# Kernel tuning notes

Measured on AMD Instinct MI355X. Metric: run time of the kernel, lower is better.

## Reference

```python
import jax, jax.numpy as jnp
import numpy as np

B, T, E, H = 16, 4096, 64, 8
K, GADD, RADD, REGION = 256, 8, 8, 64
MIN_SIGMA, SIGMA_SCALE, SIGMA_BOOST = 0.05, 1.0, 2.0
VS = K * (4 + GADD + RADD)


def setup_inputs() -> dict:
    key = jax.random.key(0)
    ks = jax.random.split(key, 10)
    return {
        "x": jax.random.normal(ks[0], (B, T, E), jnp.float32),
        "Wq": jax.random.normal(ks[1], (E, E * H), jnp.float32) / np.float32(np.sqrt(E)),
        "Wk": jax.random.normal(ks[2], (E, E * H), jnp.float32) / np.float32(np.sqrt(E)),
        "Wv": jax.random.normal(ks[3], (E, E * H), jnp.float32) / np.float32(np.sqrt(E)),
        "Wu": jax.random.normal(ks[4], (H * E, E), jnp.float32) / np.float32(np.sqrt(H * E)),
        "bu": jnp.zeros((E,), jnp.float32),
        "means_p": jax.random.normal(ks[5], (K, 2), jnp.float32),
        "sigmas_p": jax.random.normal(ks[6], (K,), jnp.float32),
        "global_ints": jax.random.randint(ks[7], (B, 1, K, GADD, 2), 0, T, jnp.int32),
        "local_offsets": jax.random.randint(ks[8], (B, 1, K, RADD, 2), 0, REGION, jnp.int32),
    }


def _flip(x):
    # util.flip: sort each (i, j) pair so row >= col (below-diagonal / causal)
    hi = jnp.max(x, axis=-1, keepdims=True)
    lo = jnp.min(x, axis=-1, keepdims=True)
    return jnp.concatenate([hi, lo], axis=-1)


def _forward(x, Wq, Wk, Wv, Wu, bu, means_p, sigmas_p, global_ints, local_offsets):
    b, t, e = x.shape
    h, k = H, K

    # ---- hyper(): continuous means/sigmas over the (t, t) attention matrix
    means = jnp.broadcast_to(means_p[None, None], (b, 1, k, 2))
    means = _flip(means)
    means = jax.nn.sigmoid(means) * (t - 1)                       # (b,1,k,2) in [0, t-1]
    sig = jax.nn.softplus(sigmas_p + SIGMA_BOOST) + MIN_SIGMA     # (k,)
    sigmas = jnp.broadcast_to((sig * t * SIGMA_SCALE)[None, None, :, None], (b, 1, k, 2))

    # ---- ngenerate: 2^rank floor/ceil neighbours + global + relative-window samples
    fl, ce = jnp.floor(means), jnp.ceil(means)
    pat = jnp.array([[0., 0.], [0., 1.], [1., 0.], [1., 1.]], jnp.float32)  # (4,2)
    neigh = fl[:, :, :, None, :] * (1.0 - pat) + ce[:, :, :, None, :] * pat
    neigh = jnp.clip(neigh, 0, t - 1).astype(jnp.int32)           # (b,1,k,4,2)
    lower = jnp.clip(jnp.floor(means) - REGION // 2, 0, t - REGION).astype(jnp.int32)
    local = lower[:, :, :, None, :] + local_offsets               # (b,1,k,RADD,2)
    idx = jnp.concatenate([neigh, global_ints, local], axis=3).reshape(b, 1, VS, 2)
    idx = _flip(idx)                                              # (b,1,VS,2), row >= col

    # ---- densities: unnormalized Gaussian weight of each int tuple under each point
    indfl = idx.astype(jnp.float32)
    diff = (indfl[:, :, :, None, :] - means[:, :, None, :, :]) / sigmas[:, :, None, :, :]
    props = jnp.exp(-0.5 * jnp.sum(diff * diff, axis=-1))         # (b,1,VS,K)

    # ---- nduplicates: zero all-but-one of identical index tuples per batch
    ids = idx[:, 0, :, 0] * t + idx[:, 0, :, 1]                   # (b, VS)
    def dupmask(v):
        o = jnp.argsort(v)
        s = v[o]
        d = jnp.concatenate([jnp.zeros((1,), bool), s[1:] == s[:-1]])
        return jnp.zeros((VS,), bool).at[o].set(d)
    dups = jax.vmap(dupmask)(ids)                                  # (b, VS)
    props = jnp.where(dups[:, None, :, None], 0.0, props)
    props = props / jnp.sum(props, axis=2, keepdims=True)
    weights = jnp.sum(props, axis=3)                               # mvalues == 1 -> (b,1,VS)

    # ---- Q/K/V projections, per-head dim = e
    scale = e ** -0.25
    q = (x @ Wq).reshape(b, t, h, e).transpose(0, 2, 1, 3).reshape(b * h, t, e) * scale
    kk = (x @ Wk).reshape(b, t, h, e).transpose(0, 2, 1, 3).reshape(b * h, t, e) * scale
    v = (x @ Wv).reshape(b, t, h, e).transpose(0, 2, 1, 3).reshape(b * h, t, e)

    rows = jnp.broadcast_to(idx[:, 0, None, :, 0], (b, h, VS)).reshape(b * h, VS)
    cols = jnp.broadcast_to(idx[:, 0, None, :, 1], (b, h, VS)).reshape(b * h, VS)
    w = jnp.broadcast_to(weights[:, 0, None, :], (b, h, VS)).reshape(b * h, VS)

    sq = jnp.take_along_axis(q, rows[:, :, None], axis=1)          # (b*h, VS, e)
    sk = jnp.take_along_axis(kk, cols[:, :, None], axis=1)
    dot = w * jnp.sum(sq * sk, axis=-1)                            # (b*h, VS)

    # ---- segment (row-wise) softmax over the sparse pattern
    seg = (jnp.arange(b * h, dtype=jnp.int32)[:, None] * t + rows).reshape(-1)
    dflat = dot.reshape(-1)
    m = jax.lax.stop_gradient(jax.ops.segment_max(dflat, seg, num_segments=b * h * t))
    ex = jnp.exp(dflat - m[seg])
    ssum = jax.ops.segment_sum(ex, seg, num_segments=b * h * t)
    p = ex / ssum[seg]                                             # (b*h*VS,)

    # ---- sparse batched matmul: scatter-add p * V[col] into rows
    gathered = jnp.take_along_axis(v, cols[:, :, None], axis=1).reshape(-1, e)
    out = jax.ops.segment_sum(p[:, None] * gathered, seg, num_segments=b * h * t)
    out = out.reshape(b, h, t, e).transpose(0, 2, 1, 3).reshape(b, t, h * e)
    return out @ Wu + bu


def reference(x, Wq, Wk, Wv, Wu, bu, means_p, sigmas_p, global_ints, local_offsets):
    return _forward(x, Wq, Wk, Wv, Wu, bu, means_p, sigmas_p, global_ints, local_offsets)
```

## Files before the change

kernel.cpp:

```cpp
#include <hip/hip_runtime.h>
#include <hip/hip_bf16.h>
#include <math.h>

#define B 16
#define T 4096
#define E 64
#define H 8
#define KP 256
#define GADD 8
#define RADD 8
#define REGION 64
#define VS (KP * (4 + GADD + RADD))
#define NH (H * E)
#define NCHUNK 20
#define HSZ 16384

typedef __attribute__((ext_vector_type(8))) short bf16x8;
typedef __attribute__((ext_vector_type(4))) float f32x4;

__device__ inline ushort f2bf(float f) {
    union { __hip_bfloat16 h; ushort u; } cv;
    cv.h = __float2bfloat16(f);
    return cv.u;
}
__device__ inline float bflo(uint32_t p) { return __uint_as_float(p << 16); }
__device__ inline float bfhi(uint32_t p) { return __uint_as_float(p & 0xffff0000u); }

__global__ void k_points(const float* __restrict__ means_p, const float* __restrict__ sigmas_p,
                         float* __restrict__ meansf, float* __restrict__ sigt) {
    int k = threadIdx.x;
    if (k >= KP) return;
    float a = means_p[2 * k], b = means_p[2 * k + 1];
    float hi = fmaxf(a, b), lo = fminf(a, b);
    meansf[2 * k]     = (1.f / (1.f + expf(-hi))) * (float)(T - 1);
    meansf[2 * k + 1] = (1.f / (1.f + expf(-lo))) * (float)(T - 1);
    float sp = sigmas_p[k] + 2.0f;
    float s = (sp > 20.f) ? sp : log1pf(expf(sp));
    sigt[k] = (s + 0.05f) * (float)T;
}

__global__ void k_wvu(const float* __restrict__ Wv, const float* __restrict__ Wu,
                      float* __restrict__ Wvu) {
    int idx = blockIdx.x * blockDim.x + threadIdx.x;
    if (idx >= E * NH) return;
    int i = idx / NH, c = idx % NH;
    int h = c / E, j = c % E;
    float acc = 0.f;
    for (int d = 0; d < E; ++d)
        acc += Wv[i * NH + h * E + d] * Wu[(h * E + d) * E + j];
    Wvu[i * NH + c] = acc;
}

__global__ void k_prep_x(const float* __restrict__ x, ushort* __restrict__ xb) {
    int i = (blockIdx.x * 256 + threadIdx.x) * 8;
    float4 a = *(const float4*)(x + i);
    float4 b = *(const float4*)(x + i + 4);
    uint4 r;
    r.x = (uint32_t)f2bf(a.x) | ((uint32_t)f2bf(a.y) << 16);
    r.y = (uint32_t)f2bf(a.z) | ((uint32_t)f2bf(a.w) << 16);
    r.z = (uint32_t)f2bf(b.x) | ((uint32_t)f2bf(b.y) << 16);
    r.w = (uint32_t)f2bf(b.z) | ((uint32_t)f2bf(b.w) << 16);
    *(uint4*)(xb + i) = r;
}

__global__ void k_prep_w(const float* __restrict__ Wq, const float* __restrict__ Wk,
                         const float* __restrict__ Wvu, ushort* __restrict__ wfrag) {
    int t = blockIdx.x * 256 + threadIdx.x;
    if (t >= 3 * 32 * 2 * 64) return;
    int lane = t & 63, kf = (t >> 6) & 1, nf = (t >> 7) & 31, z = t >> 12;
    const float* W = (z == 0) ? Wq : (z == 1) ? Wk : Wvu;
    int col = nf * 16 + (lane & 15);
    int krow = kf * 32 + (lane >> 4) * 8;
    uint4 r;
    uint32_t v[8];
    #pragma unroll
    for (int j = 0; j < 8; ++j) v[j] = f2bf(W[(size_t)(krow + j) * NH + col]);
    r.x = v[0] | (v[1] << 16); r.y = v[2] | (v[3] << 16);
    r.z = v[4] | (v[5] << 16); r.w = v[6] | (v[7] << 16);
    *(uint4*)(wfrag + (size_t)t * 8) = r;
}

__global__ __launch_bounds__(256) void k_proj(const ushort* __restrict__ xb,
        const ushort* __restrict__ wfrag,
        __hip_bfloat16* __restrict__ q, __hip_bfloat16* __restrict__ kk,
        __hip_bfloat16* __restrict__ vu) {
    int z = blockIdx.y;
    __hip_bfloat16* outp = (z == 0) ? q : (z == 1) ? kk : vu;
    int row0 = blockIdx.x * 64;
    int wv = threadIdx.x >> 6, lane = threadIdx.x & 63;
    int arow = lane & 15, akoff = (lane >> 4) * 8;

    bf16x8 bfr[8][2];
    #pragma unroll
    for (int nf = 0; nf < 8; ++nf) {
        size_t base = ((size_t)((z * 32 + wv * 8 + nf) * 2) * 64 + lane) * 8;
        bfr[nf][0] = *(const bf16x8*)(wfrag + base);
        bfr[nf][1] = *(const bf16x8*)(wfrag + base + 64 * 8);
    }

    #pragma unroll
    for (int mf = 0; mf < 4; ++mf) {
        bf16x8 a0 = *(const bf16x8*)(xb + (size_t)(row0 + mf * 16 + arow) * 64 + akoff);
        bf16x8 a1 = *(const bf16x8*)(xb + (size_t)(row0 + mf * 16 + arow) * 64 + 32 + akoff);
        f32x4 acc[8];
        #pragma unroll
        for (int nf = 0; nf < 8; ++nf) {
            f32x4 t = {0.f, 0.f, 0.f, 0.f};
            t = __builtin_amdgcn_mfma_f32_16x16x32_bf16(a0, bfr[nf][0], t, 0, 0, 0);
            t = __builtin_amdgcn_mfma_f32_16x16x32_bf16(a1, bfr[nf][1], t, 0, 0, 0);
            acc[nf] = t;
        }
        int rbase = row0 + mf * 16 + (lane >> 4) * 4;
        #pragma unroll
        for (int rg = 0; rg < 4; ++rg) {
            uint4 o;
            o.x = (uint32_t)f2bf(acc[0][rg]) | ((uint32_t)f2bf(acc[1][rg]) << 16);
            o.y = (uint32_t)f2bf(acc[2][rg]) | ((uint32_t)f2bf(acc[3][rg]) << 16);
            o.z = (uint32_t)f2bf(acc[4][rg]) | ((uint32_t)f2bf(acc[5][rg]) << 16);
            o.w = (uint32_t)f2bf(acc[6][rg]) | ((uint32_t)f2bf(acc[7][rg]) << 16);
            *(uint4*)((ushort*)outp + (size_t)(rbase + rg) * NH + wv * 128 + (lane & 15) * 8) = o;
        }
    }
}

__global__ void k_build_idx(const int* __restrict__ g_ints, const int* __restrict__ l_offs,
                            const float* __restrict__ meansf,
                            int* __restrict__ idxrow, int* __restrict__ idxcol,
                            int* __restrict__ hkey, int* __restrict__ hval) {
    int b = blockIdx.y;
    int s = blockIdx.x * 256 + threadIdx.x;
    int* keys = hkey + b * HSZ;
    int* vals = hval + b * HSZ;
    int k = s / 20, slot = s % 20;
    float m0 = meansf[2 * k], m1 = meansf[2 * k + 1];
    int i0, i1;
    if (slot < 4) {
        float a  = (slot & 2) ? ceilf(m0) : floorf(m0);
        float bb = (slot & 1) ? ceilf(m1) : floorf(m1);
        a  = fminf(fmaxf(a, 0.f), (float)(T - 1));
        bb = fminf(fmaxf(bb, 0.f), (float)(T - 1));
        i0 = (int)a; i1 = (int)bb;
    } else if (slot < 12) {
        const int* p = g_ints + ((size_t)((b * KP + k) * GADD) + (slot - 4)) * 2;
        i0 = p[0]; i1 = p[1];
    } else {
        int lo0 = (int)fminf(fmaxf(floorf(m0) - (float)(REGION / 2), 0.f), (float)(T - REGION));
        int lo1 = (int)fminf(fmaxf(floorf(m1) - (float)(REGION / 2), 0.f), (float)(T - REGION));
        const int* p = l_offs + ((size_t)((b * KP + k) * RADD) + (slot - 12)) * 2;
        i0 = lo0 + p[0]; i1 = lo1 + p[1];
    }
    int row = max(i0, i1), col = min(i0, i1);
    idxrow[b * VS + s] = row;
    idxcol[b * VS + s] = col;
    int id = row * T + col;
    unsigned h = ((unsigned)id * 2654435761u) >> 18;
    while (true) {
        int old = atomicCAS(&keys[h], -1, id);
        if (old == -1 || old == id) { atomicMin(&vals[h], s); break; }
        h = (h + 1) & (HSZ - 1);
    }
}

__global__ __launch_bounds__(256) void k_local(const int* __restrict__ idxrow,
        const int* __restrict__ idxcol, const int* __restrict__ hkey,
        const int* __restrict__ hval, int* __restrict__ lrank, int* __restrict__ dup,
        int* __restrict__ chist) {
    int b = blockIdx.y, chunk = blockIdx.x;
    int tid = threadIdx.x;
    int s = chunk * 256 + tid;
    int r = idxrow[b * VS + s];
    int c = idxcol[b * VS + s];
    __shared__ int srow[256];
    srow[tid] = r;
    __syncthreads();
    int lr = 0;
    #pragma unroll 8
    for (int t = 0; t < 256; ++t) {
        int rt = srow[t];
        lr += (t < tid && rt == r);
    }
    lrank[b * VS + s] = lr;
    atomicAdd(&chist[(size_t)(b * T + r) * NCHUNK + chunk], 1);
    const int* keys = hkey + b * HSZ;
    const int* vals = hval + b * HSZ;
    int id = r * T + c;
    unsigned h = ((unsigned)id * 2654435761u) >> 18;
    while (keys[h] != id) h = (h + 1) & (HSZ - 1);
    dup[b * VS + s] = (vals[h] != s);
}

__global__ void k_chunkscan(int* __restrict__ chist, int* __restrict__ rowcnt) {
    int idx = blockIdx.x * 256 + threadIdx.x;
    int* p = chist + (size_t)idx * NCHUNK;
    int acc = 0;
    #pragma unroll
    for (int c = 0; c < NCHUNK; ++c) { int v = p[c]; p[c] = acc; acc += v; }
    rowcnt[idx] = acc;
}

__global__ void k_colsum(const int* __restrict__ idxrow, const int* __restrict__ idxcol,
                         const int* __restrict__ dup, const float* __restrict__ meansf,
                         const float* __restrict__ sigt, float* __restrict__ colsum) {
    int k = blockIdx.x, b = blockIdx.y;
    float m0 = meansf[2 * k], m1 = meansf[2 * k + 1];
    float inv = 1.f / sigt[k];
    float acc = 0.f;
    for (int s = threadIdx.x; s < VS; s += 256) {
        if (!dup[b * VS + s]) {
            float d0 = ((float)idxrow[b * VS + s] - m0) * inv;
            float d1 = ((float)idxcol[b * VS + s] - m1) * inv;
            acc += __expf(-0.5f * (d0 * d0 + d1 * d1));
        }
    }
    __shared__ float red[256];
    red[threadIdx.x] = acc;
    __syncthreads();
    for (int o = 128; o > 0; o >>= 1) {
        if (threadIdx.x < o) red[threadIdx.x] += red[threadIdx.x + o];
        __syncthreads();
    }
    if (threadIdx.x == 0) colsum[b * KP + k] = red[0];
}

__global__ void k_weights(const int* __restrict__ idxrow, const int* __restrict__ idxcol,
                          const int* __restrict__ dup, const float* __restrict__ meansf,
                          const float* __restrict__ sigt, const float* __restrict__ colsum,
                          float* __restrict__ wts) {
    int b = blockIdx.y;
    int s = blockIdx.x * 256 + threadIdx.x;
    __shared__ float sm[2 * KP], ss[KP], rc[KP];
    for (int k = threadIdx.x; k < KP; k += 256) {
        sm[2 * k] = meansf[2 * k];
        sm[2 * k + 1] = meansf[2 * k + 1];
        ss[k] = 1.f / sigt[k];
        rc[k] = 1.f / colsum[b * KP + k];
    }
    __syncthreads();
    float w = 0.f;
    if (!dup[b * VS + s]) {
        float r = (float)idxrow[b * VS + s], c = (float)idxcol[b * VS + s];
        #pragma unroll 4
        for (int k = 0; k < KP; ++k) {
            float d0 = (r - sm[2 * k]) * ss[k];
            float d1 = (c - sm[2 * k + 1]) * ss[k];
            w += __expf(-0.5f * (d0 * d0 + d1 * d1)) * rc[k];
        }
    }
    wts[b * VS + s] = w;
}

__global__ __launch_bounds__(1024) void k_scan(const int* __restrict__ rowcnt, int* __restrict__ rowptr) {
    int b = blockIdx.x, tid = threadIdx.x;
    __shared__ int part[1024];
    int v[4]; int loc = 0;
    for (int j = 0; j < 4; ++j) { v[j] = rowcnt[b * T + tid * 4 + j]; loc += v[j]; }
    part[tid] = loc;
    __syncthreads();
    for (int off = 1; off < 1024; off <<= 1) {
        int t = (tid >= off) ? part[tid - off] : 0;
        __syncthreads();
        part[tid] += t;
        __syncthreads();
    }
    int excl = part[tid] - loc;
    for (int j = 0; j < 4; ++j) { rowptr[b * (T + 1) + tid * 4 + j] = excl; excl += v[j]; }
    if (tid == 1023) rowptr[b * (T + 1) + T] = part[1023];
}

__global__ void k_scatter(const int* __restrict__ idxrow, const int* __restrict__ idxcol,
                          const float* __restrict__ wts, const int* __restrict__ lrank,
                          const int* __restrict__ chist, const int* __restrict__ rowptr,
                          int* __restrict__ scol, float* __restrict__ sw) {
    int b = blockIdx.y;
    int s = blockIdx.x * 256 + threadIdx.x;
    int r = idxrow[b * VS + s];
    int pos = rowptr[b * (T + 1) + r] + chist[(size_t)(b * T + r) * NCHUNK + (s >> 8)]
            + lrank[b * VS + s];
    scol[b * VS + pos] = idxcol[b * VS + s];
    sw[b * VS + pos] = wts[b * VS + s];
}

__global__ __launch_bounds__(256) void k_attn(
        const __hip_bfloat16* __restrict__ q, const __hip_bfloat16* __restrict__ kk,
        const __hip_bfloat16* __restrict__ vu, const int* __restrict__ rowptr,
        const int* __restrict__ scol, const float* __restrict__ sw,
        const float* __restrict__ bu, float* __restrict__ out) {
    int gr = blockIdx.x * 4 + (threadIdx.x >> 6);
    int b = gr >> 12;
    int r = gr & (T - 1);
    int lane = threadIdx.x & 63;
    int p0 = rowptr[b * (T + 1) + r], p1 = rowptr[b * (T + 1) + r + 1];

    uint4 q4 = *(const uint4*)((const ushort*)q + (size_t)gr * NH + lane * 8);
    float qv[8] = { bflo(q4.x), bfhi(q4.x), bflo(q4.y), bfhi(q4.y),
                    bflo(q4.z), bfhi(q4.z), bflo(q4.w), bfhi(q4.w) };

    float m0 = -INFINITY, s0 = 0.f, m1 = -INFINITY, s1 = 0.f;
    float av[8] = {0.f,0.f,0.f,0.f,0.f,0.f,0.f,0.f};

    for (int e = p0; e < p1; ++e) {
        int c = scol[b * VS + e];
        float w = sw[b * VS + e];
        size_t off = ((size_t)(b * T + c)) * NH + lane * 8;
        uint4 k4 = *(const uint4*)((const ushort*)kk + off);
        float dp0 = qv[0]*bflo(k4.x) + qv[1]*bfhi(k4.x) + qv[2]*bflo(k4.y) + qv[3]*bfhi(k4.y);
        float dp1 = qv[4]*bflo(k4.z) + qv[5]*bfhi(k4.z) + qv[6]*bflo(k4.w) + qv[7]*bfhi(k4.w);
        dp0 += __shfl_xor(dp0, 1);
        dp0 += __shfl_xor(dp0, 2);
        dp0 += __shfl_xor(dp0, 4);
        dp0 += __shfl_xor(dp0, 8);
        dp1 += __shfl_xor(dp1, 1);
        dp1 += __shfl_xor(dp1, 2);
        dp1 += __shfl_xor(dp1, 4);
        dp1 += __shfl_xor(dp1, 8);
        float d0 = 0.125f * w * dp0;
        float d1 = 0.125f * w * dp1;
        uint4 v4 = *(const uint4*)((const ushort*)vu + off);
        float vf[8] = { bflo(v4.x), bfhi(v4.x), bflo(v4.y), bfhi(v4.y),
                        bflo(v4.z), bfhi(v4.z), bflo(v4.w), bfhi(v4.w) };
        float nm0 = fmaxf(m0, d0), c0 = __expf(m0 - nm0), t0 = __expf(d0 - nm0);
        float nm1 = fmaxf(m1, d1), c1 = __expf(m1 - nm1), t1 = __expf(d1 - nm1);
        s0 = s0 * c0 + t0; m0 = nm0;
        s1 = s1 * c1 + t1; m1 = nm1;
        #pragma unroll
        for (int u = 0; u < 4; ++u) av[u] = av[u] * c0 + t0 * vf[u];
        #pragma unroll
        for (int u = 4; u < 8; ++u) av[u] = av[u] * c1 + t1 * vf[u];
    }

    float i0 = (p1 > p0) ? (1.f / s0) : 0.f;
    float i1 = (p1 > p0) ? (1.f / s1) : 0.f;
    float res[4];
    #pragma unroll
    for (int u = 0; u < 4; ++u) {
        float v = av[u] * i0 + av[u + 4] * i1;
        v += __shfl_xor(v, 16);
        v += __shfl_xor(v, 32);
        res[u] = v;
    }
    if (lane < 16) {
        #pragma unroll
        for (int u = 0; u < 4; ++u)
            out[(size_t)gr * E + u * 16 + lane] = res[u] + bu[u * 16 + lane];
    }
}

extern "C" void kernel_launch(void* const* d_in, const int* in_sizes, int n_in,
                              void* d_out, int out_size, void* d_ws, size_t ws_size,
                              hipStream_t stream) {
    const float* x        = (const float*)d_in[0];
    const float* Wq       = (const float*)d_in[1];
    const float* Wk       = (const float*)d_in[2];
    const float* Wv       = (const float*)d_in[3];
    const float* Wu       = (const float*)d_in[4];
    const float* bu       = (const float*)d_in[5];
    const float* means_p  = (const float*)d_in[6];
    const float* sigmas_p = (const float*)d_in[7];
    const int*   g_ints   = (const int*)d_in[8];
    const int*   l_offs   = (const int*)d_in[9];
    float* out = (float*)d_out;

    char* ws = (char*)d_ws;
    size_t o = 0;
    auto alloc = [&](size_t bytes) -> void* {
        void* p = ws + o;
        o += (bytes + 255) & ~(size_t)255;
        return p;
    };
    __hip_bfloat16* q   = (__hip_bfloat16*)alloc((size_t)B * T * NH * 2);
    __hip_bfloat16* kk  = (__hip_bfloat16*)alloc((size_t)B * T * NH * 2);
    __hip_bfloat16* vu  = (__hip_bfloat16*)alloc((size_t)B * T * NH * 2);
    ushort* xb    = (ushort*)alloc((size_t)B * T * E * 2);
    ushort* wfrag = (ushort*)alloc((size_t)3 * 32 * 2 * 64 * 8 * 2);
    float* Wvu    = (float*)alloc((size_t)E * NH * 4);
    float* meansf = (float*)alloc(KP * 2 * 4);
    float* sigt   = (float*)alloc(KP * 4);
    int*   idxrow = (int*)alloc((size_t)B * VS * 4);
    int*   idxcol = (int*)alloc((size_t)B * VS * 4);
    float* wts    = (float*)alloc((size_t)B * VS * 4);
    int*   lrank  = (int*)alloc((size_t)B * VS * 4);
    int*   dup    = (int*)alloc((size_t)B * VS * 4);
    float* colsum = (float*)alloc((size_t)B * KP * 4);
    int*   rowcnt = (int*)alloc((size_t)B * T * 4);
    int*   rowptr = (int*)alloc((size_t)B * (T + 1) * 4);
    int*   scol   = (int*)alloc((size_t)B * VS * 4);
    float* sw     = (float*)alloc((size_t)B * VS * 4);
    int*   hkey   = (int*)alloc((size_t)B * HSZ * 4);
    int*   hval   = (int*)alloc((size_t)B * HSZ * 4);
    int*   chist  = (int*)alloc((size_t)B * T * NCHUNK * 4);

    hipMemsetAsync(hkey, 0xFF, (size_t)B * HSZ * 4, stream);
    hipMemsetAsync(hval, 0x7F, (size_t)B * HSZ * 4, stream);
    hipMemsetAsync(chist, 0, (size_t)B * T * NCHUNK * 4, stream);

    k_points<<<1, 256, 0, stream>>>(means_p, sigmas_p, meansf, sigt);
    k_wvu<<<(E * NH + 255) / 256, 256, 0, stream>>>(Wv, Wu, Wvu);
    k_prep_x<<<(B * T * E / 8) / 256, 256, 0, stream>>>(x, xb);
    k_prep_w<<<(3 * 32 * 2 * 64 + 255) / 256, 256, 0, stream>>>(Wq, Wk, Wvu, wfrag);
    k_build_idx<<<dim3(VS / 256, B), 256, 0, stream>>>(g_ints, l_offs, meansf, idxrow, idxcol, hkey, hval);
    k_local<<<dim3(NCHUNK, B), 256, 0, stream>>>(idxrow, idxcol, hkey, hval, lrank, dup, chist);
    k_chunkscan<<<B * T / 256, 256, 0, stream>>>(chist, rowcnt);
    k_colsum<<<dim3(KP, B), 256, 0, stream>>>(idxrow, idxcol, dup, meansf, sigt, colsum);
    k_weights<<<dim3(VS / 256, B), 256, 0, stream>>>(idxrow, idxcol, dup, meansf, sigt, colsum, wts);
    k_scan<<<B, 1024, 0, stream>>>(rowcnt, rowptr);
    k_scatter<<<dim3(VS / 256, B), 256, 0, stream>>>(idxrow, idxcol, wts, lrank, chist, rowptr, scol, sw);
    k_proj<<<dim3(B * T / 64, 3), 256, 0, stream>>>(xb, wfrag, q, kk, vu);
    k_attn<<<B * T / 4, 256, 0, stream>>>(q, kk, vu, rowptr, scol, sw, bu, out);
}
```

Baseline: 183.7 us.

## Fuse prep kernels into consumers and swizzle attention block order

```diff
diff --git a/kernel.cpp b/kernel.cpp
--- a/kernel.cpp
+++ b/kernel.cpp
@@ -25,106 +25,98 @@
 }
 __device__ inline float bflo(uint32_t p) { return __uint_as_float(p << 16); }
 __device__ inline float bfhi(uint32_t p) { return __uint_as_float(p & 0xffff0000u); }
-
-__global__ void k_points(const float* __restrict__ means_p, const float* __restrict__ sigmas_p,
-                         float* __restrict__ meansf, float* __restrict__ sigt) {
-    int k = threadIdx.x;
-    if (k >= KP) return;
-    float a = means_p[2 * k], b = means_p[2 * k + 1];
-    float hi = fmaxf(a, b), lo = fminf(a, b);
-    meansf[2 * k]     = (1.f / (1.f + expf(-hi))) * (float)(T - 1);
-    meansf[2 * k + 1] = (1.f / (1.f + expf(-lo))) * (float)(T - 1);
-    float sp = sigmas_p[k] + 2.0f;
-    float s = (sp > 20.f) ? sp : log1pf(expf(sp));
-    sigt[k] = (s + 0.05f) * (float)T;
-}
-
-__global__ void k_wvu(const float* __restrict__ Wv, const float* __restrict__ Wu,
-                      float* __restrict__ Wvu) {
-    int idx = blockIdx.x * blockDim.x + threadIdx.x;
-    if (idx >= E * NH) return;
-    int i = idx / NH, c = idx % NH;
-    int h = c / E, j = c % E;
-    float acc = 0.f;
-    for (int d = 0; d < E; ++d)
-        acc += Wv[i * NH + h * E + d] * Wu[(h * E + d) * E + j];
-    Wvu[i * NH + c] = acc;
-}
-
-__global__ void k_prep_x(const float* __restrict__ x, ushort* __restrict__ xb) {
-    int i = (blockIdx.x * 256 + threadIdx.x) * 8;
-    float4 a = *(const float4*)(x + i);
-    float4 b = *(const float4*)(x + i + 4);
-    uint4 r;
-    r.x = (uint32_t)f2bf(a.x) | ((uint32_t)f2bf(a.y) << 16);
-    r.y = (uint32_t)f2bf(a.z) | ((uint32_t)f2bf(a.w) << 16);
-    r.z = (uint32_t)f2bf(b.x) | ((uint32_t)f2bf(b.y) << 16);
-    r.w = (uint32_t)f2bf(b.z) | ((uint32_t)f2bf(b.w) << 16);
-    *(uint4*)(xb + i) = r;
-}
+__device__ inline float sigm(float v) { return 1.f / (1.f + expf(-v)); }
 
 __global__ void k_prep_w(const float* __restrict__ Wq, const float* __restrict__ Wk,
-                         const float* __restrict__ Wvu, ushort* __restrict__ wfrag) {
+                         const float* __restrict__ Wv, const float* __restrict__ Wu,
+                         ushort* __restrict__ wfrag) {
     int t = blockIdx.x * 256 + threadIdx.x;
     if (t >= 3 * 32 * 2 * 64) return;
     int lane = t & 63, kf = (t >> 6) & 1, nf = (t >> 7) & 31, z = t >> 12;
-    const float* W = (z == 0) ? Wq : (z == 1) ? Wk : Wvu;
     int col = nf * 16 + (lane & 15);
     int krow = kf * 32 + (lane >> 4) * 8;
+    uint32_t v[8];
+    if (z < 2) {
+        const float* W = (z == 0) ? Wq : Wk;
+        #pragma unroll
+        for (int j = 0; j < 8; ++j) v[j] = f2bf(W[(size_t)(krow + j) * NH + col]);
+    } else {
+        int h = col >> 6, jc = col & 63;
+        #pragma unroll
+        for (int j = 0; j < 8; ++j) {
+            const float* wvrow = Wv + (size_t)(krow + j) * NH + h * 64;
+            const float* wucol = Wu + (size_t)h * 64 * 64 + jc;
+            float acc = 0.f;
+            for (int d = 0; d < 64; ++d) acc += wvrow[d] * wucol[d * 64];
+            v[j] = f2bf(acc);
+        }
+    }
     uint4 r;
-    uint32_t v[8];
-    #pragma unroll
-    for (int j = 0; j < 8; ++j) v[j] = f2bf(W[(size_t)(krow + j) * NH + col]);
     r.x = v[0] | (v[1] << 16); r.y = v[2] | (v[3] << 16);
     r.z = v[4] | (v[5] << 16); r.w = v[6] | (v[7] << 16);
     *(uint4*)(wfrag + (size_t)t * 8) = r;
 }
 
-__global__ __launch_bounds__(256) void k_proj(const ushort* __restrict__ xb,
+__global__ __launch_bounds__(256) void k_proj(const float* __restrict__ x,
         const ushort* __restrict__ wfrag,
         __hip_bfloat16* __restrict__ q, __hip_bfloat16* __restrict__ kk,
         __hip_bfloat16* __restrict__ vu) {
-    int z = blockIdx.y;
-    __hip_bfloat16* outp = (z == 0) ? q : (z == 1) ? kk : vu;
     int row0 = blockIdx.x * 64;
     int wv = threadIdx.x >> 6, lane = threadIdx.x & 63;
     int arow = lane & 15, akoff = (lane >> 4) * 8;
 
-    bf16x8 bfr[8][2];
+    bf16x8 a[4][2];
     #pragma unroll
-    for (int nf = 0; nf < 8; ++nf) {
-        size_t base = ((size_t)((z * 32 + wv * 8 + nf) * 2) * 64 + lane) * 8;
-        bfr[nf][0] = *(const bf16x8*)(wfrag + base);
-        bfr[nf][1] = *(const bf16x8*)(wfrag + base + 64 * 8);
-    }
+    for (int mf = 0; mf < 4; ++mf)
+        #pragma unroll
+        for (int kf = 0; kf < 2; ++kf) {
+            const float* p = x + (size_t)(row0 + mf * 16 + arow) * 64 + kf * 32 + akoff;
+            float4 fa = *(const float4*)p;
+            float4 fb = *(const float4*)(p + 4);
+            union { bf16x8 v; uint32_t u[4]; } cv;
+            cv.u[0] = (uint32_t)f2bf(fa.x) | ((uint32_t)f2bf(fa.y) << 16);
+            cv.u[1] = (uint32_t)f2bf(fa.z) | ((uint32_t)f2bf(fa.w) << 16);
+            cv.u[2] = (uint32_t)f2bf(fb.x) | ((uint32_t)f2bf(fb.y) << 16);
+            cv.u[3] = (uint32_t)f2bf(fb.z) | ((uint32_t)f2bf(fb.w) << 16);
+            a[mf][kf] = cv.v;
+        }
 
     #pragma unroll
-    for (int mf = 0; mf < 4; ++mf) {
-        bf16x8 a0 = *(const bf16x8*)(xb + (size_t)(row0 + mf * 16 + arow) * 64 + akoff);
-        bf16x8 a1 = *(const bf16x8*)(xb + (size_t)(row0 + mf * 16 + arow) * 64 + 32 + akoff);
-        f32x4 acc[8];
+    for (int z = 0; z < 3; ++z) {
+        __hip_bfloat16* outp = (z == 0) ? q : (z == 1) ? kk : vu;
+        bf16x8 b0[8], b1[8];
         #pragma unroll
         for (int nf = 0; nf < 8; ++nf) {
-            f32x4 t = {0.f, 0.f, 0.f, 0.f};
-            t = __builtin_amdgcn_mfma_f32_16x16x32_bf16(a0, bfr[nf][0], t, 0, 0, 0);
-            t = __builtin_amdgcn_mfma_f32_16x16x32_bf16(a1, bfr[nf][1], t, 0, 0, 0);
-            acc[nf] = t;
-        }
-        int rbase = row0 + mf * 16 + (lane >> 4) * 4;
-        #pragma unroll
-        for (int rg = 0; rg < 4; ++rg) {
-            uint4 o;
-            o.x = (uint32_t)f2bf(acc[0][rg]) | ((uint32_t)f2bf(acc[1][rg]) << 16);
-            o.y = (uint32_t)f2bf(acc[2][rg]) | ((uint32_t)f2bf(acc[3][rg]) << 16);
-            o.z = (uint32_t)f2bf(acc[4][rg]) | ((uint32_t)f2bf(acc[5][rg]) << 16);
-            o.w = (uint32_t)f2bf(acc[6][rg]) | ((uint32_t)f2bf(acc[7][rg]) << 16);
-            *(uint4*)((ushort*)outp + (size_t)(rbase + rg) * NH + wv * 128 + (lane & 15) * 8) = o;
+            size_t base = ((size_t)((z * 32 + wv * 8 + nf) * 2) * 64 + lane) * 8;
+            b0[nf] = *(const bf16x8*)(wfrag + base);
+            b1[nf] = *(const bf16x8*)(wfrag + base + 64 * 8);
+        }
+        #pragma unroll
+        for (int mf = 0; mf < 4; ++mf) {
+            f32x4 acc[8];
+            #pragma unroll
+            for (int nf = 0; nf < 8; ++nf) {
+                f32x4 t = {0.f, 0.f, 0.f, 0.f};
+                t = __builtin_amdgcn_mfma_f32_16x16x32_bf16(a[mf][0], b0[nf], t, 0, 0, 0);
+                t = __builtin_amdgcn_mfma_f32_16x16x32_bf16(a[mf][1], b1[nf], t, 0, 0, 0);
+                acc[nf] = t;
+            }
+            int rbase = row0 + mf * 16 + (lane >> 4) * 4;
+            #pragma unroll
+            for (int rg = 0; rg < 4; ++rg) {
+                uint4 o;
+                o.x = (uint32_t)f2bf(acc[0][rg]) | ((uint32_t)f2bf(acc[1][rg]) << 16);
+                o.y = (uint32_t)f2bf(acc[2][rg]) | ((uint32_t)f2bf(acc[3][rg]) << 16);
+                o.z = (uint32_t)f2bf(acc[4][rg]) | ((uint32_t)f2bf(acc[5][rg]) << 16);
+                o.w = (uint32_t)f2bf(acc[6][rg]) | ((uint32_t)f2bf(acc[7][rg]) << 16);
+                *(uint4*)((ushort*)outp + (size_t)(rbase + rg) * NH + wv * 128 + (lane & 15) * 8) = o;
+            }
         }
     }
 }
 
 __global__ void k_build_idx(const int* __restrict__ g_ints, const int* __restrict__ l_offs,
-                            const float* __restrict__ meansf,
+                            const float* __restrict__ means_p,
                             int* __restrict__ idxrow, int* __restrict__ idxcol,
                             int* __restrict__ hkey, int* __restrict__ hval) {
     int b = blockIdx.y;
@@ -132,7 +124,9 @@
     int* keys = hkey + b * HSZ;
     int* vals = hval + b * HSZ;
     int k = s / 20, slot = s % 20;
-    float m0 = meansf[2 * k], m1 = meansf[2 * k + 1];
+    float pa = means_p[2 * k], pb = means_p[2 * k + 1];
+    float m0 = sigm(fmaxf(pa, pb)) * (float)(T - 1);
+    float m1 = sigm(fminf(pa, pb)) * (float)(T - 1);
     int i0, i1;
     if (slot < 4) {
         float a  = (slot & 2) ? ceilf(m0) : floorf(m0);
@@ -189,21 +183,16 @@
     dup[b * VS + s] = (vals[h] != s);
 }
 
-__global__ void k_chunkscan(int* __restrict__ chist, int* __restrict__ rowcnt) {
-    int idx = blockIdx.x * 256 + threadIdx.x;
-    int* p = chist + (size_t)idx * NCHUNK;
-    int acc = 0;
-    #pragma unroll
-    for (int c = 0; c < NCHUNK; ++c) { int v = p[c]; p[c] = acc; acc += v; }
-    rowcnt[idx] = acc;
-}
-
 __global__ void k_colsum(const int* __restrict__ idxrow, const int* __restrict__ idxcol,
-                         const int* __restrict__ dup, const float* __restrict__ meansf,
-                         const float* __restrict__ sigt, float* __restrict__ colsum) {
+                         const int* __restrict__ dup, const float* __restrict__ means_p,
+                         const float* __restrict__ sigmas_p, float* __restrict__ colsum) {
     int k = blockIdx.x, b = blockIdx.y;
-    float m0 = meansf[2 * k], m1 = meansf[2 * k + 1];
-    float inv = 1.f / sigt[k];
+    float pa = means_p[2 * k], pb = means_p[2 * k + 1];
+    float m0 = sigm(fmaxf(pa, pb)) * (float)(T - 1);
+    float m1 = sigm(fminf(pa, pb)) * (float)(T - 1);
+    float sp = sigmas_p[k] + 2.0f;
+    float sg = (sp > 20.f) ? sp : log1pf(expf(sp));
+    float inv = 1.f / ((sg + 0.05f) * (float)T);
     float acc = 0.f;
     for (int s = threadIdx.x; s < VS; s += 256) {
         if (!dup[b * VS + s]) {
@@ -223,16 +212,20 @@
 }
 
 __global__ void k_weights(const int* __restrict__ idxrow, const int* __restrict__ idxcol,
-                          const int* __restrict__ dup, const float* __restrict__ meansf,
-                          const float* __restrict__ sigt, const float* __restrict__ colsum,
+                          const int* __restrict__ dup, const float* __restrict__ means_p,
+                          const float* __restrict__ sigmas_p, const float* __restrict__ colsum,
                           float* __restrict__ wts) {
     int b = blockIdx.y;
     int s = blockIdx.x * 256 + threadIdx.x;
     __shared__ float sm[2 * KP], ss[KP], rc[KP];
-    for (int k = threadIdx.x; k < KP; k += 256) {
-        sm[2 * k] = meansf[2 * k];
-        sm[2 * k + 1] = meansf[2 * k + 1];
-        ss[k] = 1.f / sigt[k];
+    {
+        int k = threadIdx.x;
+        float pa = means_p[2 * k], pb = means_p[2 * k + 1];
+        sm[2 * k]     = sigm(fmaxf(pa, pb)) * (float)(T - 1);
+        sm[2 * k + 1] = sigm(fminf(pa, pb)) * (float)(T - 1);
+        float sp = sigmas_p[k] + 2.0f;
+        float sg = (sp > 20.f) ? sp : log1pf(expf(sp));
+        ss[k] = 1.f / ((sg + 0.05f) * (float)T);
         rc[k] = 1.f / colsum[b * KP + k];
     }
     __syncthreads();
@@ -249,11 +242,19 @@
     wts[b * VS + s] = w;
 }
 
-__global__ __launch_bounds__(1024) void k_scan(const int* __restrict__ rowcnt, int* __restrict__ rowptr) {
+__global__ __launch_bounds__(1024) void k_scan(int* __restrict__ chist, int* __restrict__ rowptr) {
     int b = blockIdx.x, tid = threadIdx.x;
     __shared__ int part[1024];
     int v[4]; int loc = 0;
-    for (int j = 0; j < 4; ++j) { v[j] = rowcnt[b * T + tid * 4 + j]; loc += v[j]; }
+    #pragma unroll
+    for (int j = 0; j < 4; ++j) {
+        int row = tid * 4 + j;
+        int* p = chist + (size_t)(b * T + row) * NCHUNK;
+        int acc = 0;
+        #pragma unroll
+        for (int c = 0; c < NCHUNK; ++c) { int t = p[c]; p[c] = acc; acc += t; }
+        v[j] = acc; loc += acc;
+    }
     part[tid] = loc;
     __syncthreads();
     for (int off = 1; off < 1024; off <<= 1) {
@@ -263,6 +264,7 @@
         __syncthreads();
     }
     int excl = part[tid] - loc;
+    #pragma unroll
     for (int j = 0; j < 4; ++j) { rowptr[b * (T + 1) + tid * 4 + j] = excl; excl += v[j]; }
     if (tid == 1023) rowptr[b * (T + 1) + T] = part[1023];
 }
@@ -285,7 +287,9 @@
         const __hip_bfloat16* __restrict__ vu, const int* __restrict__ rowptr,
         const int* __restrict__ scol, const float* __restrict__ sw,
         const float* __restrict__ bu, float* __restrict__ out) {
-    int gr = blockIdx.x * 4 + (threadIdx.x >> 6);
+    int bid = blockIdx.x;
+    int swz = ((bid & 7) << 11) | (bid >> 3);
+    int gr = swz * 4 + (threadIdx.x >> 6);
     int b = gr >> 12;
     int r = gr & (T - 1);
     int lane = threadIdx.x & 63;
@@ -370,18 +374,13 @@
     __hip_bfloat16* q   = (__hip_bfloat16*)alloc((size_t)B * T * NH * 2);
     __hip_bfloat16* kk  = (__hip_bfloat16*)alloc((size_t)B * T * NH * 2);
     __hip_bfloat16* vu  = (__hip_bfloat16*)alloc((size_t)B * T * NH * 2);
-    ushort* xb    = (ushort*)alloc((size_t)B * T * E * 2);
     ushort* wfrag = (ushort*)alloc((size_t)3 * 32 * 2 * 64 * 8 * 2);
-    float* Wvu    = (float*)alloc((size_t)E * NH * 4);
-    float* meansf = (float*)alloc(KP * 2 * 4);
-    float* sigt   = (float*)alloc(KP * 4);
     int*   idxrow = (int*)alloc((size_t)B * VS * 4);
     int*   idxcol = (int*)alloc((size_t)B * VS * 4);
     float* wts    = (float*)alloc((size_t)B * VS * 4);
     int*   lrank  = (int*)alloc((size_t)B * VS * 4);
     int*   dup    = (int*)alloc((size_t)B * VS * 4);
     float* colsum = (float*)alloc((size_t)B * KP * 4);
-    int*   rowcnt = (int*)alloc((size_t)B * T * 4);
     int*   rowptr = (int*)alloc((size_t)B * (T + 1) * 4);
     int*   scol   = (int*)alloc((size_t)B * VS * 4);
     float* sw     = (float*)alloc((size_t)B * VS * 4);
@@ -393,17 +392,13 @@
     hipMemsetAsync(hval, 0x7F, (size_t)B * HSZ * 4, stream);
     hipMemsetAsync(chist, 0, (size_t)B * T * NCHUNK * 4, stream);
 
-    k_points<<<1, 256, 0, stream>>>(means_p, sigmas_p, meansf, sigt);
-    k_wvu<<<(E * NH + 255) / 256, 256, 0, stream>>>(Wv, Wu, Wvu);
-    k_prep_x<<<(B * T * E / 8) / 256, 256, 0, stream>>>(x, xb);
-    k_prep_w<<<(3 * 32 * 2 * 64 + 255) / 256, 256, 0, stream>>>(Wq, Wk, Wvu, wfrag);
-    k_build_idx<<<dim3(VS / 256, B), 256, 0, stream>>>(g_ints, l_offs, meansf, idxrow, idxcol, hkey, hval);
+    k_prep_w<<<(3 * 32 * 2 * 64 + 255) / 256, 256, 0, stream>>>(Wq, Wk, Wv, Wu, wfrag);
+    k_build_idx<<<dim3(VS / 256, B), 256, 0, stream>>>(g_ints, l_offs, means_p, idxrow, idxcol, hkey, hval);
     k_local<<<dim3(NCHUNK, B), 256, 0, stream>>>(idxrow, idxcol, hkey, hval, lrank, dup, chist);
-    k_chunkscan<<<B * T / 256, 256, 0, stream>>>(chist, rowcnt);
-    k_colsum<<<dim3(KP, B), 256, 0, stream>>>(idxrow, idxcol, dup, meansf, sigt, colsum);
-    k_weights<<<dim3(VS / 256, B), 256, 0, stream>>>(idxrow, idxcol, dup, meansf, sigt, colsum, wts);
-    k_scan<<<B, 1024, 0, stream>>>(rowcnt, rowptr);
+    k_colsum<<<dim3(KP, B), 256, 0, stream>>>(idxrow, idxcol, dup, means_p, sigmas_p, colsum);
+    k_weights<<<dim3(VS / 256, B), 256, 0, stream>>>(idxrow, idxcol, dup, means_p, sigmas_p, colsum, wts);
+    k_scan<<<B, 1024, 0, stream>>>(chist, rowptr);
     k_scatter<<<dim3(VS / 256, B), 256, 0, stream>>>(idxrow, idxcol, wts, lrank, chist, rowptr, scol, sw);
-    k_proj<<<dim3(B * T / 64, 3), 256, 0, stream>>>(xb, wfrag, q, kk, vu);
+    k_proj<<<B * T / 64, 256, 0, stream>>>(x, wfrag, q, kk, vu);
     k_attn<<<B * T / 4, 256, 0, stream>>>(q, kk, vu, rowptr, scol, sw, bu, out);
 }
```

After: 202.6 us. +10.2%, slower.
